# Kernel tuning notes

Hardware: AMD Instinct MI355X
Metric: run time of the kernel (lower is better)

The kernel has to match this reference:

```python
import jax, jax.numpy as jnp
import numpy as np

B, C = 20000, 8          # trees, children (leaves) per tree
WORD, TAG, MEM = 300, 50, 150


def gru_cell(x, h, w_ih, w_hh, b_ih, b_hh):
    # torch.nn.GRUCell math; gate order r, z, n
    gi = x @ w_ih.T + b_ih
    gh = h @ w_hh.T + b_hh
    ir, iz, i_n = jnp.split(gi, 3, axis=-1)
    hr, hz, hn = jnp.split(gh, 3, axis=-1)
    r = jax.nn.sigmoid(ir + hr)
    z = jax.nn.sigmoid(iz + hz)
    n = jnp.tanh(i_n + r * hn)
    return (1.0 - z) * n + z * h


def setup_inputs() -> dict:
    key = jax.random.key(0)
    ks = jax.random.split(key, 16)
    s = 0.05  # small init scale for weights
    return {
        "embs": jax.random.normal(ks[0], (B, C, WORD), jnp.float32),
        "tags": jax.random.normal(ks[1], (B, C, TAG), jnp.float32),
        "tag_parent": jax.random.normal(ks[2], (B, TAG), jnp.float32),
        "w_ih_leaf": jax.random.normal(ks[3], (3 * MEM, WORD + TAG), jnp.float32) * s,
        "w_hh_leaf": jax.random.normal(ks[4], (3 * MEM, MEM), jnp.float32) * s,
        "b_ih_leaf": jax.random.normal(ks[5], (3 * MEM,), jnp.float32) * s,
        "b_hh_leaf": jax.random.normal(ks[6], (3 * MEM,), jnp.float32) * s,
        "w_ih_child": jax.random.normal(ks[7], (3 * MEM, MEM + 2 * TAG), jnp.float32) * s,
        "w_hh_child": jax.random.normal(ks[8], (3 * MEM, MEM), jnp.float32) * s,
        "b_ih_child": jax.random.normal(ks[9], (3 * MEM,), jnp.float32) * s,
        "b_hh_child": jax.random.normal(ks[10], (3 * MEM,), jnp.float32) * s,
        "w_ih_node": jax.random.normal(ks[11], (3 * MEM, 1), jnp.float32) * s,
        "w_hh_node": jax.random.normal(ks[12], (3 * MEM, MEM), jnp.float32) * s,
        "b_ih_node": jax.random.normal(ks[13], (3 * MEM,), jnp.float32) * s,
        "b_hh_node": jax.random.normal(ks[14], (3 * MEM,), jnp.float32) * s,
    }


def reference(embs, tags, tag_parent,
              w_ih_leaf, w_hh_leaf, b_ih_leaf, b_hh_leaf,
              w_ih_child, w_hh_child, b_ih_child, b_hh_child,
              w_ih_node, w_hh_node, b_ih_node, b_hh_node):
    # 1) all leaves at once: GRUCell(concat(word, tag), h=0)  -> [B, C, MEM]
    x_leaf = jnp.concatenate([embs, tags], axis=-1)            # [B, C, WORD+TAG]
    h0 = jnp.zeros((B, C, MEM), x_leaf.dtype)
    leaf_h = gru_cell(x_leaf, h0, w_ih_leaf, w_hh_leaf, b_ih_leaf, b_hh_leaf)

    # 2) child inputs: concat(child state, child tag, parent tag)  -> [B, C, MEM+2*TAG]
    tp = jnp.broadcast_to(tag_parent[:, None, :], (B, C, TAG))
    x_child = jnp.concatenate([leaf_h, tags, tp], axis=-1)

    # 3) sequential left-to-right fold over children with children GRUCell
    def step(h, x_i):
        h_new = gru_cell(x_i, h, w_ih_child, w_hh_child, b_ih_child, b_hh_child)
        return h_new, None

    h_init = jnp.zeros((B, MEM), x_leaf.dtype)
    h_final, _ = jax.lax.scan(step, h_init, jnp.swapaxes(x_child, 0, 1))  # scan over C

    # 4) node GRUCell with x = zeros(1)
    x_zeros = jnp.zeros((B, 1), x_leaf.dtype)
    root = gru_cell(x_zeros, h_final, w_ih_node, w_hh_node, b_ih_node, b_hh_node)
    return root  # [B, MEM]
```

## Files before the change

kernel.cpp:

```cpp
#include <hip/hip_runtime.h>


typedef _Float16 f16;
typedef _Float16 f16x4 __attribute__((ext_vector_type(4)));
typedef _Float16 f16x8 __attribute__((ext_vector_type(8)));
typedef float f32x4 __attribute__((ext_vector_type(4)));

namespace {

constexpr int NTREE = 20000;
constexpr int CCH   = 8;
constexpr int WORD  = 300;
constexpr int TAGD  = 50;
constexpr int MEMD  = 150;
constexpr int NBLK  = 250;
constexpr int LBLK  = 313;

constexpr int KT_L = 11;
constexpr int KT_I = 8;
constexpr int KT_H = 5;
constexpr int KT_N = 5;
constexpr int NTILE = 30;

constexpr size_t OFF_WL   = 0;
constexpr size_t OFF_WI   = OFF_WL + (size_t)KT_L * NTILE * 64 * 16;
constexpr size_t OFF_WH   = OFF_WI + (size_t)KT_I * NTILE * 64 * 16;
constexpr size_t OFF_WN   = OFF_WH + (size_t)KT_H * NTILE * 64 * 16;
constexpr size_t OFF_BIAS = OFF_WN + (size_t)KT_N * NTILE * 64 * 16;
constexpr size_t OFF_DATA = OFF_BIAS + 16 * 160 * 4;

constexpr size_t TG_BYTES = 15360;
constexpr size_t C_STRIDE = (size_t)1250 * TG_BYTES;
constexpr size_t GI_BYTES = (size_t)CCH * C_STRIDE;
constexpr size_t WS_R3    = OFF_DATA + GI_BYTES;
constexpr int    HW_S  = 152;
constexpr size_t WS_R2 = OFF_DATA + (size_t)CCH * NTREE * HW_S * 2;


__device__ __forceinline__ float sigmoid_f(float x) {
  return 1.0f / (1.0f + __expf(-x));
}
__device__ __forceinline__ float tanh_f(float x) {
  float ax = fabsf(x);
  float e  = __expf(-2.0f * ax);
  float t  = (1.0f - e) / (1.0f + e);
  return copysignf(t, x);
}

__global__ void prep_kernel(const float* __restrict__ w_ih_leaf,
                            const float* __restrict__ b_ih_leaf,
                            const float* __restrict__ b_hh_leaf,
                            const float* __restrict__ w_ih_child,
                            const float* __restrict__ w_hh_child,
                            const float* __restrict__ b_ih_child,
                            const float* __restrict__ b_hh_child,
                            const float* __restrict__ w_hh_node,
                            const float* __restrict__ b_ih_node,
                            const float* __restrict__ b_hh_node,
                            char* __restrict__ ws) {
  const int NWL = KT_L * NTILE * 64;
  const int NWI = KT_I * NTILE * 64;
  const int NWH = KT_H * NTILE * 64;
  const int NWN = KT_N * NTILE * 64;
  int t = blockIdx.x * blockDim.x + threadIdx.x;

  if (t < NWL) {
    int kt = t / (NTILE * 64), rem = t % (NTILE * 64);
    int nt = rem / 64, l = rem % 64;
    int gate = nt / 10, jt = nt % 10;
    int j = jt * 16 + (l & 15);
    bool valid = j < MEMD;
    int g = gate * MEMD + (valid ? j : 0);
    f16x8 v;
#pragma unroll
    for (int e = 0; e < 8; ++e) {
      int k = kt * 32 + ((l >> 4) * 8) + e;
      v[e] = (f16)((valid && k < WORD + TAGD) ? w_ih_leaf[g * (WORD + TAGD) + k] : 0.0f);
    }
    ((f16x8*)(ws + OFF_WL))[t] = v;
    return;
  }
  t -= NWL;
  if (t < NWI) {
    int kt = t / (NTILE * 64), rem = t % (NTILE * 64);
    int nt = rem / 64, l = rem % 64;
    int gate = nt / 10, jt = nt % 10;
    int j = jt * 16 + (l & 15);
    bool valid = j < MEMD;
    int g = gate * MEMD + (valid ? j : 0);
    f16x8 v;
#pragma unroll
    for (int e = 0; e < 8; ++e) {
      int k = kt * 32 + ((l >> 4) * 8) + e;
      int src = (k < 150) ? k : (k >= 152 && k < 252) ? (k - 2) : -1;
      v[e] = (f16)((valid && src >= 0) ? w_ih_child[g * 250 + src] : 0.0f);
    }
    ((f16x8*)(ws + OFF_WI))[t] = v;
    return;
  }
  t -= NWI;
  if (t < NWH) {
    int kt = t / (NTILE * 64), rem = t % (NTILE * 64);
    int nt = rem / 64, l = rem % 64;
    int gate = nt / 10, jt = nt % 10;
    int j = jt * 16 + (l & 15);
    bool valid = j < MEMD;
    int g = gate * MEMD + (valid ? j : 0);
    f16x8 v;
#pragma unroll
    for (int e = 0; e < 8; ++e) {
      int k = kt * 32 + ((l >> 4) * 8) + e;
      v[e] = (f16)((valid && k < MEMD) ? w_hh_child[g * MEMD + k] : 0.0f);
    }
    ((f16x8*)(ws + OFF_WH))[t] = v;
    return;
  }
  t -= NWH;
  if (t < NWN) {
    int kt = t / (NTILE * 64), rem = t % (NTILE * 64);
    int nt = rem / 64, l = rem % 64;
    int gate = nt / 10, jt = nt % 10;
    int j = jt * 16 + (l & 15);
    bool valid = j < MEMD;
    int g = gate * MEMD + (valid ? j : 0);
    f16x8 v;
#pragma unroll
    for (int e = 0; e < 8; ++e) {
      int k = kt * 32 + ((l >> 4) * 8) + e;
      v[e] = (f16)((valid && k < MEMD) ? w_hh_node[g * MEMD + k] : 0.0f);
    }
    ((f16x8*)(ws + OFF_WN))[t] = v;
    return;
  }
  t -= NWN;
  if (t < 16 * 160) {
    int arr = t / 160, j = t % 160;
    float v = 0.0f;
    if (j < MEMD) {
      switch (arr) {
        case 0:  v = b_ih_leaf[j] + b_hh_leaf[j]; break;
        case 1:  v = b_ih_leaf[MEMD + j] + b_hh_leaf[MEMD + j]; break;
        case 2:  v = b_ih_leaf[2 * MEMD + j]; break;
        case 3:  v = b_hh_leaf[2 * MEMD + j]; break;
        case 4:  v = b_ih_child[j] + b_hh_child[j]; break;
        case 5:  v = b_ih_child[MEMD + j] + b_hh_child[MEMD + j]; break;
        case 6:  v = b_ih_child[2 * MEMD + j]; break;
        case 7:  v = b_hh_child[2 * MEMD + j]; break;
        case 8:  v = b_ih_node[j] + b_hh_node[j]; break;
        case 9:  v = b_ih_node[MEMD + j] + b_hh_node[MEMD + j]; break;
        case 10: v = b_ih_node[2 * MEMD + j]; break;
        case 11: v = b_hh_node[2 * MEMD + j]; break;
        case 12: v = b_ih_child[j]; break;
        case 13: v = b_ih_child[MEMD + j]; break;
        case 14: v = b_hh_child[j]; break;
        case 15: v = b_hh_child[MEMD + j]; break;
      }
    }
    ((float*)(ws + OFF_BIAS))[arr * 160 + j] = v;
  }
}

__global__ __launch_bounds__(640, 1)
void leaf9_kernel(const float* __restrict__ embs,
                  const float* __restrict__ tags,
                  const float* __restrict__ tag_parent,
                  char* __restrict__ ws) {
  __shared__ f16 buf[64 * 360];
  f16* xle = buf;
  f16* xch = buf;

  const f16x8* WL   = (const f16x8*)(ws + OFF_WL);
  const f16x8* WI   = (const f16x8*)(ws + OFF_WI);
  const float* BIAS = (const float*)(ws + OFF_BIAS);

  const int tid = threadIdx.x, lane = tid & 63, w = tid >> 6;
  const int blk = blockIdx.x, c = blockIdx.y, t0 = blk * 64;
  const int arow = lane & 15, acol8 = (lane >> 4) * 8, qrow = (lane >> 4) * 4;
  const int j = w * 16 + arow;
  const bool jok = j < MEMD;

  for (int i = tid; i < 64 * 75; i += 640) {
    int r = i / 75, k4 = i - r * 75;
    int row = min(t0 + r, NTREE - 1);
    float4 v = *(const float4*)(embs + ((size_t)row * CCH + c) * WORD + 4 * k4);
    f16* p = xle + r * 360 + 4 * k4;
    p[0] = (f16)v.x; p[1] = (f16)v.y; p[2] = (f16)v.z; p[3] = (f16)v.w;
  }
  for (int i = tid; i < 64 * 25; i += 640) {
    int r = i / 25, k2 = i - r * 25;
    int row = min(t0 + r, NTREE - 1);
    float2 v = *(const float2*)(tags + ((size_t)row * CCH + c) * TAGD + 2 * k2);
    xle[r * 360 + 300 + 2 * k2]     = (f16)v.x;
    xle[r * 360 + 300 + 2 * k2 + 1] = (f16)v.y;
  }
  if (tid < 64) {
    xle[tid * 360 + 350] = (f16)0.0f;
    xle[tid * 360 + 351] = (f16)0.0f;
  }
  __syncthreads();

  f32x4 acc[3][4];
#pragma unroll
  for (int g = 0; g < 3; ++g)
#pragma unroll
    for (int m = 0; m < 4; ++m) acc[g][m] = 0.f;

  {
    f16x8 bcur[3], bnxt[3];
#pragma unroll
    for (int g = 0; g < 3; ++g) bcur[g] = WL[(g * 10 + w) * 64 + lane];
    for (int kt = 0; kt < KT_L; ++kt) {
      if (kt + 1 < KT_L) {
#pragma unroll
        for (int g = 0; g < 3; ++g)
          bnxt[g] = WL[((kt + 1) * NTILE + g * 10 + w) * 64 + lane];
      }
      f16x8 a0 = *(const f16x8*)(xle + kt * 32 + acol8 + (arow)      * 360);
      f16x8 a1 = *(const f16x8*)(xle + kt * 32 + acol8 + (16 + arow) * 360);
      f16x8 a2 = *(const f16x8*)(xle + kt * 32 + acol8 + (32 + arow) * 360);
      f16x8 a3 = *(const f16x8*)(xle + kt * 32 + acol8 + (48 + arow) * 360);
#pragma unroll
      for (int g = 0; g < 3; ++g) {
        acc[g][0] = __builtin_amdgcn_mfma_f32_16x16x32_f16(a0, bcur[g], acc[g][0], 0, 0, 0);
        acc[g][1] = __builtin_amdgcn_mfma_f32_16x16x32_f16(a1, bcur[g], acc[g][1], 0, 0, 0);
        acc[g][2] = __builtin_amdgcn_mfma_f32_16x16x32_f16(a2, bcur[g], acc[g][2], 0, 0, 0);
        acc[g][3] = __builtin_amdgcn_mfma_f32_16x16x32_f16(a3, bcur[g], acc[g][3], 0, 0, 0);
      }
#pragma unroll
      for (int g = 0; g < 3; ++g) bcur[g] = bnxt[g];
    }
  }
  __syncthreads();

  {
    const float bLr = BIAS[j], bLz = BIAS[160 + j];
    const float bLi = BIAS[320 + j], bLh = BIAS[480 + j];
#pragma unroll
    for (int m = 0; m < 4; ++m)
#pragma unroll
      for (int q = 0; q < 4; ++q) {
        int row = 16 * m + qrow + q;
        float rg = sigmoid_f(acc[0][m][q] + bLr);
        float zg = sigmoid_f(acc[1][m][q] + bLz);
        float ng = tanh_f(acc[2][m][q] + bLi + rg * bLh);
        if (jok) xch[row * 264 + j] = (f16)((1.0f - zg) * ng);
      }
  }
  for (int i = tid; i < 64 * 25; i += 640) {
    int r = i / 25, k2 = i - r * 25;
    int row = min(t0 + r, NTREE - 1);
    float2 v = *(const float2*)(tags + ((size_t)row * CCH + c) * TAGD + 2 * k2);
    xch[r * 264 + 152 + 2 * k2] = (f16)v.x;
    xch[r * 264 + 153 + 2 * k2] = (f16)v.y;
  }
  for (int i = tid; i < 64 * 25; i += 640) {
    int r = i / 25, k2 = i - r * 25;
    int row = min(t0 + r, NTREE - 1);
    float2 v = *(const float2*)(tag_parent + (size_t)row * TAGD + 2 * k2);
    xch[r * 264 + 202 + 2 * k2] = (f16)v.x;
    xch[r * 264 + 203 + 2 * k2] = (f16)v.y;
  }
  for (int i = tid; i < 64 * 6; i += 640) {
    int r = i / 6, k = i - r * 6;
    int col = (k < 2) ? (150 + k) : (250 + k);
    xch[r * 264 + col] = (f16)0.0f;
  }
  __syncthreads();

#pragma unroll
  for (int g = 0; g < 3; ++g)
#pragma unroll
    for (int m = 0; m < 4; ++m) acc[g][m] = 0.f;

  {
    f16x8 bcur[3], bnxt[3];
#pragma unroll
    for (int g = 0; g < 3; ++g) bcur[g] = WI[(g * 10 + w) * 64 + lane];
    for (int kt = 0; kt < KT_I; ++kt) {
      if (kt + 1 < KT_I) {
#pragma unroll
        for (int g = 0; g < 3; ++g)
          bnxt[g] = WI[((kt + 1) * NTILE + g * 10 + w) * 64 + lane];
      }
      f16x8 a0 = *(const f16x8*)(xch + kt * 32 + acol8 + (arow)      * 264);
      f16x8 a1 = *(const f16x8*)(xch + kt * 32 + acol8 + (16 + arow) * 264);
      f16x8 a2 = *(const f16x8*)(xch + kt * 32 + acol8 + (32 + arow) * 264);
      f16x8 a3 = *(const f16x8*)(xch + kt * 32 + acol8 + (48 + arow) * 264);
#pragma unroll
      for (int g = 0; g < 3; ++g) {
        acc[g][0] = __builtin_amdgcn_mfma_f32_16x16x32_f16(a0, bcur[g], acc[g][0], 0, 0, 0);
        acc[g][1] = __builtin_amdgcn_mfma_f32_16x16x32_f16(a1, bcur[g], acc[g][1], 0, 0, 0);
        acc[g][2] = __builtin_amdgcn_mfma_f32_16x16x32_f16(a2, bcur[g], acc[g][2], 0, 0, 0);
        acc[g][3] = __builtin_amdgcn_mfma_f32_16x16x32_f16(a3, bcur[g], acc[g][3], 0, 0, 0);
      }
#pragma unroll
      for (int g = 0; g < 3; ++g) bcur[g] = bnxt[g];
    }
  }

  {
    const float bi[3] = {BIAS[12 * 160 + j], BIAS[13 * 160 + j], BIAS[6 * 160 + j]};
#pragma unroll
    for (int m = 0; m < 4; ++m) {
      if (t0 + 16 * m < NTREE) {
        int tg = blk * 4 + m;
        char* base = ws + OFF_DATA + (size_t)c * C_STRIDE + (size_t)tg * TG_BYTES +
                     (size_t)lane * 8;
#pragma unroll
        for (int g = 0; g < 3; ++g) {
          f16x4 v;
#pragma unroll
          for (int q = 0; q < 4; ++q) v[q] = (f16)(acc[g][m][q] + bi[g]);
          *(f16x4*)(base + (size_t)(g * 10 + w) * 512) = v;
        }
      }
    }
  }
}

__global__ __launch_bounds__(640, 1)
void fold6_kernel(const char* __restrict__ ws,
                  float* __restrict__ out) {
  __shared__ f16 hls[80 * 168];

  const f16x8* WH   = (const f16x8*)(ws + OFF_WH);
  const f16x8* WN   = (const f16x8*)(ws + OFF_WN);
  const float* BIAS = (const float*)(ws + OFF_BIAS);

  const int tid = threadIdx.x, lane = tid & 63, w = tid >> 6;
  const int blk = blockIdx.x, t0 = blk * 80;
  const int arow = lane & 15, acol8 = (lane >> 4) * 8, qrow = (lane >> 4) * 4;
  const int j = w * 16 + arow;
  const bool jok = j < MEMD;

  const float bhr = BIAS[14 * 160 + j], bhz = BIAS[15 * 160 + j], bhn = BIAS[7 * 160 + j];
  const float bNr = BIAS[8 * 160 + j],  bNz = BIAS[9 * 160 + j];
  const float bNi = BIAS[10 * 160 + j], bNh = BIAS[11 * 160 + j];

  for (int i = tid; i < 80 * 18; i += 640) {
    int r = i / 18;
    hls[r * 168 + 150 + (i - r * 18)] = (f16)0.0f;
  }

  f16x8 whr[5], whz[5], whn[5];
#pragma unroll
  for (int kt = 0; kt < KT_H; ++kt) {
    whr[kt] = WH[(kt * NTILE + w) * 64 + lane];
    whz[kt] = WH[(kt * NTILE + 10 + w) * 64 + lane];
    whn[kt] = WH[(kt * NTILE + 20 + w) * 64 + lane];
  }

  const char* gbase = ws + OFF_DATA + (size_t)(blk * 5) * TG_BYTES +
                      (size_t)w * 512 + (size_t)lane * 8;

  f32x4 hp[5];
#pragma unroll
  for (int m = 0; m < 5; ++m) hp[m] = 0.f;

#pragma unroll
  for (int c = 0; c < CCH; ++c) {
    f16x4 gbuf[15];
#pragma unroll
    for (int m = 0; m < 5; ++m)
#pragma unroll
      for (int g = 0; g < 3; ++g)
        gbuf[m * 3 + g] = *(const f16x4*)(gbase + (size_t)c * C_STRIDE +
                                          (size_t)m * TG_BYTES + (size_t)g * 5120);

    f32x4 aR[5], aZ[5], aNh[5];
#pragma unroll
    for (int m = 0; m < 5; ++m) { aR[m] = 0.f; aZ[m] = 0.f; aNh[m] = 0.f; }

    if (c != 0) {
#pragma unroll
      for (int kt = 0; kt < KT_H; ++kt) {
        const f16* ab = hls + kt * 32 + acol8;
#pragma unroll
        for (int m = 0; m < 5; ++m) {
          f16x8 a = *(const f16x8*)(ab + (16 * m + arow) * 168);
          aR[m]  = __builtin_amdgcn_mfma_f32_16x16x32_f16(a, whr[kt], aR[m], 0, 0, 0);
          aZ[m]  = __builtin_amdgcn_mfma_f32_16x16x32_f16(a, whz[kt], aZ[m], 0, 0, 0);
          aNh[m] = __builtin_amdgcn_mfma_f32_16x16x32_f16(a, whn[kt], aNh[m], 0, 0, 0);
        }
      }
      __syncthreads();
    }

#pragma unroll
    for (int m = 0; m < 5; ++m)
#pragma unroll
      for (int q = 0; q < 4; ++q) {
        int row = 16 * m + qrow + q;
        float rg = sigmoid_f((float)gbuf[m * 3 + 0][q] + aR[m][q] + bhr);
        float zg = sigmoid_f((float)gbuf[m * 3 + 1][q] + aZ[m][q] + bhz);
        float ng = tanh_f((float)gbuf[m * 3 + 2][q] + rg * (aNh[m][q] + bhn));
        float h  = (1.0f - zg) * ng + zg * hp[m][q];
        hp[m][q] = h;
        if (jok) hls[row * 168 + j] = (f16)h;
      }
    __syncthreads();
  }

  f32x4 aR[5], aZ[5], aNh[5];
#pragma unroll
  for (int m = 0; m < 5; ++m) { aR[m] = 0.f; aZ[m] = 0.f; aNh[m] = 0.f; }
  for (int kt = 0; kt < KT_N; ++kt) {
    f16x8 br = WN[(kt * NTILE + w) * 64 + lane];
    f16x8 bz = WN[(kt * NTILE + 10 + w) * 64 + lane];
    f16x8 bn = WN[(kt * NTILE + 20 + w) * 64 + lane];
    const f16* ab = hls + kt * 32 + acol8;
#pragma unroll
    for (int m = 0; m < 5; ++m) {
      f16x8 a = *(const f16x8*)(ab + (16 * m + arow) * 168);
      aR[m]  = __builtin_amdgcn_mfma_f32_16x16x32_f16(a, br, aR[m], 0, 0, 0);
      aZ[m]  = __builtin_amdgcn_mfma_f32_16x16x32_f16(a, bz, aZ[m], 0, 0, 0);
      aNh[m] = __builtin_amdgcn_mfma_f32_16x16x32_f16(a, bn, aNh[m], 0, 0, 0);
    }
  }
#pragma unroll
  for (int m = 0; m < 5; ++m)
#pragma unroll
    for (int q = 0; q < 4; ++q) {
      int row = 16 * m + qrow + q;
      float rg = sigmoid_f(aR[m][q] + bNr);
      float zg = sigmoid_f(aZ[m][q] + bNz);
      float ng = tanh_f(bNi + rg * (aNh[m][q] + bNh));
      float o  = (1.0f - zg) * ng + zg * hp[m][q];
      if (jok) out[(size_t)(t0 + row) * MEMD + j] = o;
    }
}

namespace r2 {

__global__ __launch_bounds__(640)
void leaf_kernel(const float* __restrict__ embs,
                 const float* __restrict__ tags,
                 char* __restrict__ ws) {
  __shared__ f16 xle[80 * 360];
  const f16x8* WL   = (const f16x8*)(ws + OFF_WL);
  const float* BIAS = (const float*)(ws + OFF_BIAS);
  f16* hws = (f16*)(ws + OFF_DATA);

  const int tid = threadIdx.x, lane = tid & 63, w = tid >> 6;
  const int c = blockIdx.y, t0 = blockIdx.x * 80;
  const int arow = lane & 15, acol8 = (lane >> 4) * 8, qrow = (lane >> 4) * 4;
  const int j = w * 16 + (lane & 15);

  for (int i = tid; i < 80 * 150; i += 640) {
    int r = i / 150, k2 = i - r * 150;
    float2 v = *(const float2*)(embs + ((size_t)(t0 + r) * CCH + c) * WORD + 2 * k2);
    xle[r * 360 + 2 * k2]     = (f16)v.x;
    xle[r * 360 + 2 * k2 + 1] = (f16)v.y;
  }
  for (int i = tid; i < 80 * 25; i += 640) {
    int r = i / 25, k2 = i - r * 25;
    float2 v = *(const float2*)(tags + ((size_t)(t0 + r) * CCH + c) * TAGD + 2 * k2);
    xle[r * 360 + 300 + 2 * k2]     = (f16)v.x;
    xle[r * 360 + 300 + 2 * k2 + 1] = (f16)v.y;
  }
  for (int i = tid; i < 80; i += 640) {
    xle[i * 360 + 350] = (f16)0.0f;
    xle[i * 360 + 351] = (f16)0.0f;
  }
  __syncthreads();

  f32x4 aR[5], aZ[5], aN[5];
#pragma unroll
  for (int m = 0; m < 5; ++m) { aR[m] = 0.f; aZ[m] = 0.f; aN[m] = 0.f; }
  for (int kt = 0; kt < KT_L; ++kt) {
    f16x8 br = WL[(kt * NTILE + w) * 64 + lane];
    f16x8 bz = WL[(kt * NTILE + 10 + w) * 64 + lane];
    f16x8 bn = WL[(kt * NTILE + 20 + w) * 64 + lane];
    const f16* ab = xle + kt * 32 + acol8;
#pragma unroll
    for (int m = 0; m < 5; ++m) {
      f16x8 a = *(const f16x8*)(ab + (16 * m + arow) * 360);
      aR[m] = __builtin_amdgcn_mfma_f32_16x16x32_f16(a, br, aR[m], 0, 0, 0);
      aZ[m] = __builtin_amdgcn_mfma_f32_16x16x32_f16(a, bz, aZ[m], 0, 0, 0);
      aN[m] = __builtin_amdgcn_mfma_f32_16x16x32_f16(a, bn, aN[m], 0, 0, 0);
    }
  }
  const float bLr = BIAS[j], bLz = BIAS[160 + j], bLi = BIAS[320 + j], bLh = BIAS[480 + j];
#pragma unroll
  for (int m = 0; m < 5; ++m) {
#pragma unroll
    for (int q = 0; q < 4; ++q) {
      int row = 16 * m + qrow + q;
      float rg = sigmoid_f(aR[m][q] + bLr);
      float zg = sigmoid_f(aZ[m][q] + bLz);
      float ng = tanh_f(aN[m][q] + bLi + rg * bLh);
      float h  = (1.0f - zg) * ng;
      if (j < HW_S)
        hws[((size_t)c * NTREE + t0 + row) * HW_S + j] = (f16)(j < MEMD ? h : 0.0f);
    }
  }
}

__global__ __launch_bounds__(640)
void fold_kernel(const float* __restrict__ tags,
                 const float* __restrict__ tag_parent,
                 const char* __restrict__ ws,
                 float* __restrict__ out) {
  extern __shared__ char fsm[];
  f16* xch0 = (f16*)fsm;
  f16* xch1 = xch0 + 80 * 264;
  f16* hls  = xch1 + 80 * 264;

  const f16x8* WI   = (const f16x8*)(ws + OFF_WI);
  const f16x8* WH   = (const f16x8*)(ws + OFF_WH);
  const f16x8* WN   = (const f16x8*)(ws + OFF_WN);
  const float* BIAS = (const float*)(ws + OFF_BIAS);
  const f16*   hws  = (const f16*)(ws + OFF_DATA);

  const int tid = threadIdx.x, lane = tid & 63, w = tid >> 6;
  const int t0 = blockIdx.x * 80;
  const int arow = lane & 15, acol8 = (lane >> 4) * 8, qrow = (lane >> 4) * 4;
  const int j = w * 16 + (lane & 15);
  const bool jok = j < MEMD;

  const float bCr = BIAS[4 * 160 + j], bCz = BIAS[5 * 160 + j];
  const float bCi = BIAS[6 * 160 + j], bCh = BIAS[7 * 160 + j];
  const float bNr = BIAS[8 * 160 + j], bNz = BIAS[9 * 160 + j];
  const float bNi = BIAS[10 * 160 + j], bNh = BIAS[11 * 160 + j];

  for (int i = tid; i < 1680; i += 640) ((int4*)hls)[i] = make_int4(0, 0, 0, 0);
  for (int i = tid; i < 80 * 25; i += 640) {
    int r = i / 25, k2 = i - r * 25;
    float2 v = *(const float2*)(tag_parent + (size_t)(t0 + r) * TAGD + 2 * k2);
    f16 a = (f16)v.x, b = (f16)v.y;
    xch0[r * 264 + 202 + 2 * k2] = a; xch0[r * 264 + 203 + 2 * k2] = b;
    xch1[r * 264 + 202 + 2 * k2] = a; xch1[r * 264 + 203 + 2 * k2] = b;
  }
  for (int i = tid; i < 80 * 4; i += 640) {
    int r = i >> 2, k = i & 3;
    xch0[r * 264 + 252 + k] = (f16)0.0f;
    xch1[r * 264 + 252 + k] = (f16)0.0f;
  }
#pragma unroll
  for (int s = 0; s < 3; ++s) {
    int i = tid + 640 * s;
    if (i < 1520) {
      int r = i / 19, q = i - r * 19;
      *(f16x8*)(xch0 + r * 264 + 8 * q) =
          *(const f16x8*)(hws + ((size_t)(t0 + r)) * HW_S + 8 * q);
    }
  }
#pragma unroll
  for (int s = 0; s < 4; ++s) {
    int i = tid + 640 * s;
    if (i < 2000) {
      int r = i / 25, k2 = i - r * 25;
      float2 v = *(const float2*)(tags + ((size_t)(t0 + r) * CCH) * TAGD + 2 * k2);
      xch0[r * 264 + 152 + 2 * k2] = (f16)v.x;
      xch0[r * 264 + 153 + 2 * k2] = (f16)v.y;
    }
  }
  __syncthreads();

  f32x4 hp[5];
#pragma unroll
  for (int m = 0; m < 5; ++m) hp[m] = 0.f;

  f16* xc = xch0;
  f16* xa = xch1;

  for (int c = 0; c < CCH; ++c) {
    f16x8 ph[3];
    float2 pt[4];
    if (c < 7) {
#pragma unroll
      for (int s = 0; s < 3; ++s) {
        int i = tid + 640 * s;
        if (i < 1520) {
          int r = i / 19, q = i - r * 19;
          ph[s] = *(const f16x8*)(hws + ((size_t)(c + 1) * NTREE + t0 + r) * HW_S + 8 * q);
        }
      }
#pragma unroll
      for (int s = 0; s < 4; ++s) {
        int i = tid + 640 * s;
        if (i < 2000) {
          int r = i / 25, k2 = i - r * 25;
          pt[s] = *(const float2*)(tags + ((size_t)(t0 + r) * CCH + (c + 1)) * TAGD + 2 * k2);
        }
      }
    }

    f32x4 aR[5], aZ[5], aNi[5], aNh[5];
#pragma unroll
    for (int m = 0; m < 5; ++m) { aR[m] = 0.f; aZ[m] = 0.f; aNi[m] = 0.f; aNh[m] = 0.f; }
    for (int kt = 0; kt < KT_I; ++kt) {
      f16x8 br = WI[(kt * NTILE + w) * 64 + lane];
      f16x8 bz = WI[(kt * NTILE + 10 + w) * 64 + lane];
      f16x8 bn = WI[(kt * NTILE + 20 + w) * 64 + lane];
      const f16* ab = xc + kt * 32 + acol8;
#pragma unroll
      for (int m = 0; m < 5; ++m) {
        f16x8 a = *(const f16x8*)(ab + (16 * m + arow) * 264);
        aR[m]  = __builtin_amdgcn_mfma_f32_16x16x32_f16(a, br, aR[m], 0, 0, 0);
        aZ[m]  = __builtin_amdgcn_mfma_f32_16x16x32_f16(a, bz, aZ[m], 0, 0, 0);
        aNi[m] = __builtin_amdgcn_mfma_f32_16x16x32_f16(a, bn, aNi[m], 0, 0, 0);
      }
    }
    for (int kt = 0; kt < KT_H; ++kt) {
      f16x8 br = WH[(kt * NTILE + w) * 64 + lane];
      f16x8 bz = WH[(kt * NTILE + 10 + w) * 64 + lane];
      f16x8 bn = WH[(kt * NTILE + 20 + w) * 64 + lane];
      const f16* ab = hls + kt * 32 + acol8;
#pragma unroll
      for (int m = 0; m < 5; ++m) {
        f16x8 a = *(const f16x8*)(ab + (16 * m + arow) * 168);
        aR[m]  = __builtin_amdgcn_mfma_f32_16x16x32_f16(a, br, aR[m], 0, 0, 0);
        aZ[m]  = __builtin_amdgcn_mfma_f32_16x16x32_f16(a, bz, aZ[m], 0, 0, 0);
        aNh[m] = __builtin_amdgcn_mfma_f32_16x16x32_f16(a, bn, aNh[m], 0, 0, 0);
      }
    }
    __syncthreads();

    if (c < 7) {
#pragma unroll
      for (int s = 0; s < 3; ++s) {
        int i = tid + 640 * s;
        if (i < 1520) {
          int r = i / 19, q = i - r * 19;
          *(f16x8*)(xa + r * 264 + 8 * q) = ph[s];
        }
      }
#pragma unroll
      for (int s = 0; s < 4; ++s) {
        int i = tid + 640 * s;
        if (i < 2000) {
          int r = i / 25, k2 = i - r * 25;
          xa[r * 264 + 152 + 2 * k2] = (f16)pt[s].x;
          xa[r * 264 + 153 + 2 * k2] = (f16)pt[s].y;
        }
      }
    }

#pragma unroll
    for (int m = 0; m < 5; ++m) {
#pragma unroll
      for (int q = 0; q < 4; ++q) {
        int row = 16 * m + qrow + q;
        float rg = sigmoid_f(aR[m][q] + bCr);
        float zg = sigmoid_f(aZ[m][q] + bCz);
        float ng = tanh_f(aNi[m][q] + bCi + rg * (aNh[m][q] + bCh));
        float h  = (1.0f - zg) * ng + zg * hp[m][q];
        hp[m][q] = h;
        if (jok) hls[row * 168 + j] = (f16)h;
      }
    }
    __syncthreads();
    f16* tsw = xc; xc = xa; xa = tsw;
  }

  f32x4 aR[5], aZ[5], aNh[5];
#pragma unroll
  for (int m = 0; m < 5; ++m) { aR[m] = 0.f; aZ[m] = 0.f; aNh[m] = 0.f; }
  for (int kt = 0; kt < KT_N; ++kt) {
    f16x8 br = WN[(kt * NTILE + w) * 64 + lane];
    f16x8 bz = WN[(kt * NTILE + 10 + w) * 64 + lane];
    f16x8 bn = WN[(kt * NTILE + 20 + w) * 64 + lane];
    const f16* ab = hls + kt * 32 + acol8;
#pragma unroll
    for (int m = 0; m < 5; ++m) {
      f16x8 a = *(const f16x8*)(ab + (16 * m + arow) * 168);
      aR[m]  = __builtin_amdgcn_mfma_f32_16x16x32_f16(a, br, aR[m], 0, 0, 0);
      aZ[m]  = __builtin_amdgcn_mfma_f32_16x16x32_f16(a, bz, aZ[m], 0, 0, 0);
      aNh[m] = __builtin_amdgcn_mfma_f32_16x16x32_f16(a, bn, aNh[m], 0, 0, 0);
    }
  }
#pragma unroll
  for (int m = 0; m < 5; ++m) {
#pragma unroll
    for (int q = 0; q < 4; ++q) {
      int row = 16 * m + qrow + q;
      float rg = sigmoid_f(aR[m][q] + bNr);
      float zg = sigmoid_f(aZ[m][q] + bNz);
      float ng = tanh_f(bNi + rg * (aNh[m][q] + bNh));
      float o  = (1.0f - zg) * ng + zg * hp[m][q];
      if (jok) out[(size_t)(t0 + row) * MEMD + j] = o;
    }
  }
}

}

}

extern "C" void kernel_launch(void* const* d_in, const int* in_sizes, int n_in,
                              void* d_out, int out_size, void* d_ws, size_t ws_size,
                              hipStream_t stream) {
  const float* embs       = (const float*)d_in[0];
  const float* tags       = (const float*)d_in[1];
  const float* tag_parent = (const float*)d_in[2];
  const float* w_ih_leaf  = (const float*)d_in[3];
  const float* b_ih_leaf  = (const float*)d_in[5];
  const float* b_hh_leaf  = (const float*)d_in[6];
  const float* w_ih_child = (const float*)d_in[7];
  const float* w_hh_child = (const float*)d_in[8];
  const float* b_ih_child = (const float*)d_in[9];
  const float* b_hh_child = (const float*)d_in[10];
  const float* w_hh_node  = (const float*)d_in[12];
  const float* b_ih_node  = (const float*)d_in[13];
  const float* b_hh_node  = (const float*)d_in[14];
  float* out = (float*)d_out;
  char*  ws  = (char*)d_ws;

  prep_kernel<<<228, 256, 0, stream>>>(w_ih_leaf, b_ih_leaf, b_hh_leaf,
                                       w_ih_child, w_hh_child, b_ih_child, b_hh_child,
                                       w_hh_node, b_ih_node, b_hh_node, ws);

  if (ws_size >= WS_R3) {
    leaf9_kernel<<<dim3(LBLK, CCH), 640, 0, stream>>>(embs, tags, tag_parent, ws);
    fold6_kernel<<<NBLK, 640, 0, stream>>>(ws, out);
  } else {
    r2::leaf_kernel<<<dim3(250, CCH), 640, 0, stream>>>(embs, tags, ws);
    constexpr int FOLD_LDS = (2 * 80 * 264 + 80 * 168) * 2;
    hipFuncSetAttribute((const void*)r2::fold_kernel,
                        hipFuncAttributeMaxDynamicSharedMemorySize, FOLD_LDS);
    r2::fold_kernel<<<250, 640, FOLD_LDS, stream>>>(tags, tag_parent, ws, out);
  }
}
```

Baseline: 393.9 us.

## Fuse tag projections into leaf GEMM and double-buffer fold gate loads

The child-input GEMM is split into two parts. The tag and parent-tag part is folded into the leaf GEMM by loading tag_parent into the same shared tile and adding extra weight k-tiles (WT). The leaf-state part becomes a smaller 5-tile GEMM (WX) over a compact 168-stride buffer. This removes the second pass that reloaded tags and tag_parent and shrinks the second GEMM's K. The fold kernel now prefetches the next child's precomputed gate inputs into a double buffer, and global loads in the leaf kernel are issued into registers before the shared-memory stores. The cost is more registers for the extra accumulators and prefetch buffers, plus a larger prep kernel.

```diff
diff --git a/kernel.cpp b/kernel.cpp
--- a/kernel.cpp
+++ b/kernel.cpp
@@ -17,14 +17,21 @@
 constexpr int LBLK  = 313;
 
 constexpr int KT_L = 11;
+constexpr int KT_T = 4;
+constexpr int KT_X = 5;
 constexpr int KT_I = 8;
 constexpr int KT_H = 5;
 constexpr int KT_N = 5;
 constexpr int NTILE = 30;
 
+constexpr int XS = 424;
+constexpr int HS = 168;
+
 constexpr size_t OFF_WL   = 0;
 constexpr size_t OFF_WI   = OFF_WL + (size_t)KT_L * NTILE * 64 * 16;
-constexpr size_t OFF_WH   = OFF_WI + (size_t)KT_I * NTILE * 64 * 16;
+constexpr size_t OFF_WT   = OFF_WI + (size_t)KT_I * NTILE * 64 * 16;
+constexpr size_t OFF_WX   = OFF_WT + (size_t)KT_T * NTILE * 64 * 16;
+constexpr size_t OFF_WH   = OFF_WX + (size_t)KT_X * NTILE * 64 * 16;
 constexpr size_t OFF_WN   = OFF_WH + (size_t)KT_H * NTILE * 64 * 16;
 constexpr size_t OFF_BIAS = OFF_WN + (size_t)KT_N * NTILE * 64 * 16;
 constexpr size_t OFF_DATA = OFF_BIAS + 16 * 160 * 4;
@@ -35,7 +42,6 @@
 constexpr size_t WS_R3    = OFF_DATA + GI_BYTES;
 constexpr int    HW_S  = 152;
 constexpr size_t WS_R2 = OFF_DATA + (size_t)CCH * NTREE * HW_S * 2;
-
 
 __device__ __forceinline__ float sigmoid_f(float x) {
   return 1.0f / (1.0f + __expf(-x));
@@ -60,6 +66,8 @@
                             char* __restrict__ ws) {
   const int NWL = KT_L * NTILE * 64;
   const int NWI = KT_I * NTILE * 64;
+  const int NWT = KT_T * NTILE * 64;
+  const int NWX = KT_X * NTILE * 64;
   const int NWH = KT_H * NTILE * 64;
   const int NWN = KT_N * NTILE * 64;
   int t = blockIdx.x * blockDim.x + threadIdx.x;
@@ -99,6 +107,45 @@
     return;
   }
   t -= NWI;
+  if (t < NWT) {
+    int kt = t / (NTILE * 64), rem = t % (NTILE * 64);
+    int nt = rem / 64, l = rem % 64;
+    int gate = nt / 10, jt = nt % 10;
+    int j = jt * 16 + (l & 15);
+    bool valid = j < MEMD;
+    int g = gate * MEMD + (valid ? j : 0);
+    f16x8 v;
+#pragma unroll
+    for (int e = 0; e < 8; ++e) {
+      int k = (9 + kt) * 32 + ((l >> 4) * 8) + e;
+      float x = 0.0f;
+      if (valid) {
+        if (k >= 300 && k < 350)      x = w_ih_child[g * 250 + 150 + (k - 300)];
+        else if (k >= 352 && k < 402) x = w_ih_child[g * 250 + 200 + (k - 352)];
+      }
+      v[e] = (f16)x;
+    }
+    ((f16x8*)(ws + OFF_WT))[t] = v;
+    return;
+  }
+  t -= NWT;
+  if (t < NWX) {
+    int kt = t / (NTILE * 64), rem = t % (NTILE * 64);
+    int nt = rem / 64, l = rem % 64;
+    int gate = nt / 10, jt = nt % 10;
+    int j = jt * 16 + (l & 15);
+    bool valid = j < MEMD;
+    int g = gate * MEMD + (valid ? j : 0);
+    f16x8 v;
+#pragma unroll
+    for (int e = 0; e < 8; ++e) {
+      int k = kt * 32 + ((l >> 4) * 8) + e;
+      v[e] = (f16)((valid && k < MEMD) ? w_ih_child[g * 250 + k] : 0.0f);
+    }
+    ((f16x8*)(ws + OFF_WX))[t] = v;
+    return;
+  }
+  t -= NWX;
   if (t < NWH) {
     int kt = t / (NTILE * 64), rem = t % (NTILE * 64);
     int nt = rem / 64, l = rem % 64;
@@ -161,16 +208,17 @@
 }
 
 __global__ __launch_bounds__(640, 1)
-void leaf9_kernel(const float* __restrict__ embs,
-                  const float* __restrict__ tags,
-                  const float* __restrict__ tag_parent,
-                  char* __restrict__ ws) {
-  __shared__ f16 buf[64 * 360];
+void leaf10_kernel(const float* __restrict__ embs,
+                   const float* __restrict__ tags,
+                   const float* __restrict__ tag_parent,
+                   char* __restrict__ ws) {
+  __shared__ f16 buf[64 * XS];
   f16* xle = buf;
   f16* xch = buf;
 
   const f16x8* WL   = (const f16x8*)(ws + OFF_WL);
-  const f16x8* WI   = (const f16x8*)(ws + OFF_WI);
+  const f16x8* WT   = (const f16x8*)(ws + OFF_WT);
+  const f16x8* WX   = (const f16x8*)(ws + OFF_WX);
   const float* BIAS = (const float*)(ws + OFF_BIAS);
 
   const int tid = threadIdx.x, lane = tid & 63, w = tid >> 6;
@@ -179,55 +227,85 @@
   const int j = w * 16 + arow;
   const bool jok = j < MEMD;
 
-  for (int i = tid; i < 64 * 75; i += 640) {
-    int r = i / 75, k4 = i - r * 75;
-    int row = min(t0 + r, NTREE - 1);
-    float4 v = *(const float4*)(embs + ((size_t)row * CCH + c) * WORD + 4 * k4);
-    f16* p = xle + r * 360 + 4 * k4;
-    p[0] = (f16)v.x; p[1] = (f16)v.y; p[2] = (f16)v.z; p[3] = (f16)v.w;
-  }
-  for (int i = tid; i < 64 * 25; i += 640) {
-    int r = i / 25, k2 = i - r * 25;
-    int row = min(t0 + r, NTREE - 1);
-    float2 v = *(const float2*)(tags + ((size_t)row * CCH + c) * TAGD + 2 * k2);
-    xle[r * 360 + 300 + 2 * k2]     = (f16)v.x;
-    xle[r * 360 + 300 + 2 * k2 + 1] = (f16)v.y;
-  }
-  if (tid < 64) {
-    xle[tid * 360 + 350] = (f16)0.0f;
-    xle[tid * 360 + 351] = (f16)0.0f;
+  float4 pe[8];
+  float2 ptg[3], ptp[3];
+#pragma unroll
+  for (int s = 0; s < 8; ++s) {
+    int i = tid + 640 * s;
+    if (i < 4800) {
+      int r = i / 75, k4 = i - r * 75;
+      int row = min(t0 + r, NTREE - 1);
+      pe[s] = *(const float4*)(embs + ((size_t)row * CCH + c) * WORD + 4 * k4);
+    }
+  }
+#pragma unroll
+  for (int s = 0; s < 3; ++s) {
+    int i = tid + 640 * s;
+    if (i < 1600) {
+      int r = i / 25, k2 = i - r * 25;
+      int row = min(t0 + r, NTREE - 1);
+      ptg[s] = *(const float2*)(tags + ((size_t)row * CCH + c) * TAGD + 2 * k2);
+      ptp[s] = *(const float2*)(tag_parent + (size_t)row * TAGD + 2 * k2);
+    }
+  }
+#pragma unroll
+  for (int s = 0; s < 8; ++s) {
+    int i = tid + 640 * s;
+    if (i < 4800) {
+      int r = i / 75, k4 = i - r * 75;
+      f16* p = xle + r * XS + 4 * k4;
+      p[0] = (f16)pe[s].x; p[1] = (f16)pe[s].y; p[2] = (f16)pe[s].z; p[3] = (f16)pe[s].w;
+    }
+  }
+#pragma unroll
+  for (int s = 0; s < 3; ++s) {
+    int i = tid + 640 * s;
+    if (i < 1600) {
+      int r = i / 25, k2 = i - r * 25;
+      xle[r * XS + 300 + 2 * k2] = (f16)ptg[s].x;
+      xle[r * XS + 301 + 2 * k2] = (f16)ptg[s].y;
+      xle[r * XS + 352 + 2 * k2] = (f16)ptp[s].x;
+      xle[r * XS + 353 + 2 * k2] = (f16)ptp[s].y;
+    }
+  }
+  for (int i = tid; i < 64 * 24; i += 640) {
+    int r = i / 24, k = i - r * 24;
+    int col = (k < 2) ? (350 + k) : (400 + k);
+    xle[r * XS + col] = (f16)0.0f;
   }
   __syncthreads();
 
-  f32x4 acc[3][4];
+  f32x4 aL[3][4], aT[3][4];
 #pragma unroll
   for (int g = 0; g < 3; ++g)
 #pragma unroll
-    for (int m = 0; m < 4; ++m) acc[g][m] = 0.f;
-
-  {
-    f16x8 bcur[3], bnxt[3];
-#pragma unroll
-    for (int g = 0; g < 3; ++g) bcur[g] = WL[(g * 10 + w) * 64 + lane];
-    for (int kt = 0; kt < KT_L; ++kt) {
-      if (kt + 1 < KT_L) {
-#pragma unroll
-        for (int g = 0; g < 3; ++g)
-          bnxt[g] = WL[((kt + 1) * NTILE + g * 10 + w) * 64 + lane];
-      }
-      f16x8 a0 = *(const f16x8*)(xle + kt * 32 + acol8 + (arow)      * 360);
-      f16x8 a1 = *(const f16x8*)(xle + kt * 32 + acol8 + (16 + arow) * 360);
-      f16x8 a2 = *(const f16x8*)(xle + kt * 32 + acol8 + (32 + arow) * 360);
-      f16x8 a3 = *(const f16x8*)(xle + kt * 32 + acol8 + (48 + arow) * 360);
+    for (int m = 0; m < 4; ++m) { aL[g][m] = 0.f; aT[g][m] = 0.f; }
+
+#pragma unroll
+  for (int kt = 0; kt < 13; ++kt) {
+    f16x8 a0 = *(const f16x8*)(xle + kt * 32 + acol8 + (arow)      * XS);
+    f16x8 a1 = *(const f16x8*)(xle + kt * 32 + acol8 + (16 + arow) * XS);
+    f16x8 a2 = *(const f16x8*)(xle + kt * 32 + acol8 + (32 + arow) * XS);
+    f16x8 a3 = *(const f16x8*)(xle + kt * 32 + acol8 + (48 + arow) * XS);
+    if (kt < KT_L) {
 #pragma unroll
       for (int g = 0; g < 3; ++g) {
-        acc[g][0] = __builtin_amdgcn_mfma_f32_16x16x32_f16(a0, bcur[g], acc[g][0], 0, 0, 0);
-        acc[g][1] = __builtin_amdgcn_mfma_f32_16x16x32_f16(a1, bcur[g], acc[g][1], 0, 0, 0);
-        acc[g][2] = __builtin_amdgcn_mfma_f32_16x16x32_f16(a2, bcur[g], acc[g][2], 0, 0, 0);
-        acc[g][3] = __builtin_amdgcn_mfma_f32_16x16x32_f16(a3, bcur[g], acc[g][3], 0, 0, 0);
-      }
-#pragma unroll
-      for (int g = 0; g < 3; ++g) bcur[g] = bnxt[g];
+        f16x8 b = WL[(kt * NTILE + g * 10 + w) * 64 + lane];
+        aL[g][0] = __builtin_amdgcn_mfma_f32_16x16x32_f16(a0, b, aL[g][0], 0, 0, 0);
+        aL[g][1] = __builtin_amdgcn_mfma_f32_16x16x32_f16(a1, b, aL[g][1], 0, 0, 0);
+        aL[g][2] = __builtin_amdgcn_mfma_f32_16x16x32_f16(a2, b, aL[g][2], 0, 0, 0);
+        aL[g][3] = __builtin_amdgcn_mfma_f32_16x16x32_f16(a3, b, aL[g][3], 0, 0, 0);
+      }
+    }
+    if (kt >= 9) {
+#pragma unroll
+      for (int g = 0; g < 3; ++g) {
+        f16x8 b = WT[((kt - 9) * NTILE + g * 10 + w) * 64 + lane];
+        aT[g][0] = __builtin_amdgcn_mfma_f32_16x16x32_f16(a0, b, aT[g][0], 0, 0, 0);
+        aT[g][1] = __builtin_amdgcn_mfma_f32_16x16x32_f16(a1, b, aT[g][1], 0, 0, 0);
+        aT[g][2] = __builtin_amdgcn_mfma_f32_16x16x32_f16(a2, b, aT[g][2], 0, 0, 0);
+        aT[g][3] = __builtin_amdgcn_mfma_f32_16x16x32_f16(a3, b, aT[g][3], 0, 0, 0);
+      }
     }
   }
   __syncthreads();
@@ -240,61 +318,37 @@
 #pragma unroll
       for (int q = 0; q < 4; ++q) {
         int row = 16 * m + qrow + q;
-        float rg = sigmoid_f(acc[0][m][q] + bLr);
-        float zg = sigmoid_f(acc[1][m][q] + bLz);
-        float ng = tanh_f(acc[2][m][q] + bLi + rg * bLh);
-        if (jok) xch[row * 264 + j] = (f16)((1.0f - zg) * ng);
-      }
-  }
-  for (int i = tid; i < 64 * 25; i += 640) {
-    int r = i / 25, k2 = i - r * 25;
-    int row = min(t0 + r, NTREE - 1);
-    float2 v = *(const float2*)(tags + ((size_t)row * CCH + c) * TAGD + 2 * k2);
-    xch[r * 264 + 152 + 2 * k2] = (f16)v.x;
-    xch[r * 264 + 153 + 2 * k2] = (f16)v.y;
-  }
-  for (int i = tid; i < 64 * 25; i += 640) {
-    int r = i / 25, k2 = i - r * 25;
-    int row = min(t0 + r, NTREE - 1);
-    float2 v = *(const float2*)(tag_parent + (size_t)row * TAGD + 2 * k2);
-    xch[r * 264 + 202 + 2 * k2] = (f16)v.x;
-    xch[r * 264 + 203 + 2 * k2] = (f16)v.y;
-  }
-  for (int i = tid; i < 64 * 6; i += 640) {
-    int r = i / 6, k = i - r * 6;
-    int col = (k < 2) ? (150 + k) : (250 + k);
-    xch[r * 264 + col] = (f16)0.0f;
+        float rg = sigmoid_f(aL[0][m][q] + bLr);
+        float zg = sigmoid_f(aL[1][m][q] + bLz);
+        float ng = tanh_f(aL[2][m][q] + bLi + rg * bLh);
+        if (jok) xch[row * HS + j] = (f16)((1.0f - zg) * ng);
+      }
+  }
+  for (int i = tid; i < 64 * 18; i += 640) {
+    int r = i / 18;
+    xch[r * HS + 150 + (i - r * 18)] = (f16)0.0f;
   }
   __syncthreads();
 
+  f32x4 aX[3][4];
 #pragma unroll
   for (int g = 0; g < 3; ++g)
 #pragma unroll
-    for (int m = 0; m < 4; ++m) acc[g][m] = 0.f;
-
-  {
-    f16x8 bcur[3], bnxt[3];
-#pragma unroll
-    for (int g = 0; g < 3; ++g) bcur[g] = WI[(g * 10 + w) * 64 + lane];
-    for (int kt = 0; kt < KT_I; ++kt) {
-      if (kt + 1 < KT_I) {
-#pragma unroll
-        for (int g = 0; g < 3; ++g)
-          bnxt[g] = WI[((kt + 1) * NTILE + g * 10 + w) * 64 + lane];
-      }
-      f16x8 a0 = *(const f16x8*)(xch + kt * 32 + acol8 + (arow)      * 264);
-      f16x8 a1 = *(const f16x8*)(xch + kt * 32 + acol8 + (16 + arow) * 264);
-      f16x8 a2 = *(const f16x8*)(xch + kt * 32 + acol8 + (32 + arow) * 264);
-      f16x8 a3 = *(const f16x8*)(xch + kt * 32 + acol8 + (48 + arow) * 264);
-#pragma unroll
-      for (int g = 0; g < 3; ++g) {
-        acc[g][0] = __builtin_amdgcn_mfma_f32_16x16x32_f16(a0, bcur[g], acc[g][0], 0, 0, 0);
-        acc[g][1] = __builtin_amdgcn_mfma_f32_16x16x32_f16(a1, bcur[g], acc[g][1], 0, 0, 0);
-        acc[g][2] = __builtin_amdgcn_mfma_f32_16x16x32_f16(a2, bcur[g], acc[g][2], 0, 0, 0);
-        acc[g][3] = __builtin_amdgcn_mfma_f32_16x16x32_f16(a3, bcur[g], acc[g][3], 0, 0, 0);
-      }
-#pragma unroll
-      for (int g = 0; g < 3; ++g) bcur[g] = bnxt[g];
+    for (int m = 0; m < 4; ++m) aX[g][m] = 0.f;
+
+#pragma unroll
+  for (int kt = 0; kt < KT_X; ++kt) {
+    f16x8 a0 = *(const f16x8*)(xch + kt * 32 + acol8 + (arow)      * HS);
+    f16x8 a1 = *(const f16x8*)(xch + kt * 32 + acol8 + (16 + arow) * HS);
+    f16x8 a2 = *(const f16x8*)(xch + kt * 32 + acol8 + (32 + arow) * HS);
+    f16x8 a3 = *(const f16x8*)(xch + kt * 32 + acol8 + (48 + arow) * HS);
+#pragma unroll
+    for (int g = 0; g < 3; ++g) {
+      f16x8 b = WX[(kt * NTILE + g * 10 + w) * 64 + lane];
+      aX[g][0] = __builtin_amdgcn_mfma_f32_16x16x32_f16(a0, b, aX[g][0], 0, 0, 0);
+      aX[g][1] = __builtin_amdgcn_mfma_f32_16x16x32_f16(a1, b, aX[g][1], 0, 0, 0);
+      aX[g][2] = __builtin_amdgcn_mfma_f32_16x16x32_f16(a2, b, aX[g][2], 0, 0, 0);
+      aX[g][3] = __builtin_amdgcn_mfma_f32_16x16x32_f16(a3, b, aX[g][3], 0, 0, 0);
     }
   }
 
@@ -310,7 +364,8 @@
         for (int g = 0; g < 3; ++g) {
           f16x4 v;
 #pragma unroll
-          for (int q = 0; q < 4; ++q) v[q] = (f16)(acc[g][m][q] + bi[g]);
+          for (int q = 0; q < 4; ++q)
+            v[q] = (f16)(aT[g][m][q] + aX[g][m][q] + bi[g]);
           *(f16x4*)(base + (size_t)(g * 10 + w) * 512) = v;
         }
       }
@@ -319,9 +374,9 @@
 }
 
 __global__ __launch_bounds__(640, 1)
-void fold6_kernel(const char* __restrict__ ws,
-                  float* __restrict__ out) {
-  __shared__ f16 hls[80 * 168];
+void fold10_kernel(const char* __restrict__ ws,
+                   float* __restrict__ out) {
+  __shared__ f16 hls[80 * HS];
 
   const f16x8* WH   = (const f16x8*)(ws + OFF_WH);
   const f16x8* WN   = (const f16x8*)(ws + OFF_WN);
@@ -339,7 +394,7 @@
 
   for (int i = tid; i < 80 * 18; i += 640) {
     int r = i / 18;
-    hls[r * 168 + 150 + (i - r * 18)] = (f16)0.0f;
+    hls[r * HS + 150 + (i - r * 18)] = (f16)0.0f;
   }
 
   f16x8 whr[5], whz[5], whn[5];
@@ -353,19 +408,28 @@
   const char* gbase = ws + OFF_DATA + (size_t)(blk * 5) * TG_BYTES +
                       (size_t)w * 512 + (size_t)lane * 8;
 
+  f16x4 gbuf[2][15];
+#pragma unroll
+  for (int m = 0; m < 5; ++m)
+#pragma unroll
+    for (int g = 0; g < 3; ++g)
+      gbuf[0][m * 3 + g] = *(const f16x4*)(gbase + (size_t)m * TG_BYTES + (size_t)g * 5120);
+
   f32x4 hp[5];
 #pragma unroll
   for (int m = 0; m < 5; ++m) hp[m] = 0.f;
 
 #pragma unroll
   for (int c = 0; c < CCH; ++c) {
-    f16x4 gbuf[15];
-#pragma unroll
-    for (int m = 0; m < 5; ++m)
-#pragma unroll
-      for (int g = 0; g < 3; ++g)
-        gbuf[m * 3 + g] = *(const f16x4*)(gbase + (size_t)c * C_STRIDE +
-                                          (size_t)m * TG_BYTES + (size_t)g * 5120);
+    if (c < CCH - 1) {
+#pragma unroll
+      for (int m = 0; m < 5; ++m)
+#pragma unroll
+        for (int g = 0; g < 3; ++g)
+          gbuf[(c + 1) & 1][m * 3 + g] =
+              *(const f16x4*)(gbase + (size_t)(c + 1) * C_STRIDE +
+                              (size_t)m * TG_BYTES + (size_t)g * 5120);
+    }
 
     f32x4 aR[5], aZ[5], aNh[5];
 #pragma unroll
@@ -377,7 +441,7 @@
         const f16* ab = hls + kt * 32 + acol8;
 #pragma unroll
         for (int m = 0; m < 5; ++m) {
-          f16x8 a = *(const f16x8*)(ab + (16 * m + arow) * 168);
+          f16x8 a = *(const f16x8*)(ab + (16 * m + arow) * HS);
           aR[m]  = __builtin_amdgcn_mfma_f32_16x16x32_f16(a, whr[kt], aR[m], 0, 0, 0);
           aZ[m]  = __builtin_amdgcn_mfma_f32_16x16x32_f16(a, whz[kt], aZ[m], 0, 0, 0);
           aNh[m] = __builtin_amdgcn_mfma_f32_16x16x32_f16(a, whn[kt], aNh[m], 0, 0, 0);
@@ -391,12 +455,12 @@
 #pragma unroll
       for (int q = 0; q < 4; ++q) {
         int row = 16 * m + qrow + q;
-        float rg = sigmoid_f((float)gbuf[m * 3 + 0][q] + aR[m][q] + bhr);
-        float zg = sigmoid_f((float)gbuf[m * 3 + 1][q] + aZ[m][q] + bhz);
-        float ng = tanh_f((float)gbuf[m * 3 + 2][q] + rg * (aNh[m][q] + bhn));
+        float rg = sigmoid_f((float)gbuf[c & 1][m * 3 + 0][q] + aR[m][q] + bhr);
+        float zg = sigmoid_f((float)gbuf[c & 1][m * 3 + 1][q] + aZ[m][q] + bhz);
+        float ng = tanh_f((float)gbuf[c & 1][m * 3 + 2][q] + rg * (aNh[m][q] + bhn));
         float h  = (1.0f - zg) * ng + zg * hp[m][q];
         hp[m][q] = h;
-        if (jok) hls[row * 168 + j] = (f16)h;
+        if (jok) hls[row * HS + j] = (f16)h;
       }
     __syncthreads();
   }
@@ -411,7 +475,7 @@
     const f16* ab = hls + kt * 32 + acol8;
 #pragma unroll
     for (int m = 0; m < 5; ++m) {
-      f16x8 a = *(const f16x8*)(ab + (16 * m + arow) * 168);
+      f16x8 a = *(const f16x8*)(ab + (16 * m + arow) * HS);
       aR[m]  = __builtin_amdgcn_mfma_f32_16x16x32_f16(a, br, aR[m], 0, 0, 0);
       aZ[m]  = __builtin_amdgcn_mfma_f32_16x16x32_f16(a, bz, aZ[m], 0, 0, 0);
       aNh[m] = __builtin_amdgcn_mfma_f32_16x16x32_f16(a, bn, aNh[m], 0, 0, 0);
@@ -707,13 +771,13 @@
   float* out = (float*)d_out;
   char*  ws  = (char*)d_ws;
 
-  prep_kernel<<<228, 256, 0, stream>>>(w_ih_leaf, b_ih_leaf, b_hh_leaf,
+  prep_kernel<<<295, 256, 0, stream>>>(w_ih_leaf, b_ih_leaf, b_hh_leaf,
                                        w_ih_child, w_hh_child, b_ih_child, b_hh_child,
                                        w_hh_node, b_ih_node, b_hh_node, ws);
 
   if (ws_size >= WS_R3) {
-    leaf9_kernel<<<dim3(LBLK, CCH), 640, 0, stream>>>(embs, tags, tag_parent, ws);
-    fold6_kernel<<<NBLK, 640, 0, stream>>>(ws, out);
+    leaf10_kernel<<<dim3(LBLK, CCH), 640, 0, stream>>>(embs, tags, tag_parent, ws);
+    fold10_kernel<<<NBLK, 640, 0, stream>>>(ws, out);
   } else {
     r2::leaf_kernel<<<dim3(250, CCH), 640, 0, stream>>>(embs, tags, ws);
     constexpr int FOLD_LDS = (2 * 80 * 264 + 80 * 168) * 2;
```

Result: slower. 471.8 us (+19.8%).
